# Optimization experiments

Hardware: AMD Instinct MI355X
Metric: run time of the kernel (lower is better)

The kernel has to match this reference:

```python
import jax, jax.numpy as jnp
import numpy as np

V = 1048576        # number of leaves (power of two -> uniform tree depth)
EMB = 128
B = 65536
DEPTH = int(np.log2(V))  # 20: every leaf of the complete heap sits at depth 20


def setup_inputs() -> dict:
    key = jax.random.key(0)
    k1, k2, k3, k4 = jax.random.split(key, 4)
    emb_table = jax.random.normal(k1, (V, EMB), dtype=jnp.float32)
    hsoftmax = jax.random.uniform(k2, (V - 1, EMB), dtype=jnp.float32)  # torch.rand init
    u = jax.random.randint(k3, (B,), 0, V, dtype=jnp.int32)
    v = jax.random.randint(k4, (B,), 0, V, dtype=jnp.int32)
    return {"emb_table": emb_table, "hsoftmax": hsoftmax, "u": u, "v": v}


def _paths(u):
    """Root-to-leaf path (visited as leaf-to-root) for leaf u.
    Returns path_nodes [B, DEPTH] (inner-node indices) and
    path_signs [B, DEPTH] (+1 if we arrived as a left child, -1 otherwise)."""
    node = (V - 1) + u  # heap index of leaf; leaf_pos is the identity
    nodes, signs = [], []
    for _ in range(DEPTH):  # fixed depth: static Python loop, jit-friendly
        is_left = (node & 1) == 1
        parent = jnp.where(is_left, node >> 1, (node - 1) >> 1)
        nodes.append(parent)
        signs.append(jnp.where(is_left, 1.0, -1.0).astype(jnp.float32))
        node = parent
    return jnp.stack(nodes, axis=1), jnp.stack(signs, axis=1)


def reference(emb_table, hsoftmax, u, v):
    # v_emb: [B, E]
    v_emb = emb_table[v]
    path_nodes, path_signs = _paths(u)          # [B, D], [B, D]
    node_embs = hsoftmax[path_nodes]            # [B, D, E] gather
    dots = jnp.einsum("bde,be->bd", node_embs, v_emb)
    # left child: -log(sigmoid(s)); right child: -log(1-sigmoid(s)) = -log(sigmoid(-s))
    loss = -jnp.sum(jax.nn.log_sigmoid(path_signs * dots), axis=1)  # [B]
    return loss
```

## Files before the change

kernel.cpp:

```cpp
#include <hip/hip_runtime.h>
#include <hip/hip_bf16.h>
#include <math.h>

#define V_LEAVES 1048576
#define EMB 128
#define DEPTH 20

__global__ __launch_bounds__(256, 4) void deepwalk_hsm_kernel(
    const float* __restrict__ emb_table,
    const float* __restrict__ hsoftmax,
    const int*   __restrict__ u,
    const int*   __restrict__ v,
    float*       __restrict__ out,
    int batch)
{
    const int tid  = blockIdx.x * blockDim.x + threadIdx.x;
    const int elem = tid >> 4;
    const int sl   = tid & 15;
    if (elem >= batch) return;

    const int vi = v[elem];
    const float4* vrow = (const float4*)(emb_table + (size_t)vi * EMB);
    const float4 ve0 = vrow[sl * 2 + 0];
    const float4 ve1 = vrow[sl * 2 + 1];

    const unsigned np = (unsigned)V_LEAVES + (unsigned)u[elem];

    {
    }
    unsigned p0 = (np >> 1) - 1u;
    const float4* hrow = (const float4*)(hsoftmax + (size_t)p0 * EMB);
    float4 h0 = hrow[sl * 2 + 0];
    float4 h1 = hrow[sl * 2 + 1];

    float loss = 0.0f;

#pragma unroll 4
    for (int d = 0; d < DEPTH; ++d) {
        const float4 c0 = h0;
        const float4 c1 = h1;

        if (d + 1 < DEPTH) {
            const unsigned pn = (np >> (d + 2)) - 1u;
            const float4* nrow = (const float4*)(hsoftmax + (size_t)pn * EMB);
            h0 = nrow[sl * 2 + 0];
            h1 = nrow[sl * 2 + 1];
        }

        float p = c0.x * ve0.x + c0.y * ve0.y + c0.z * ve0.z + c0.w * ve0.w
                + c1.x * ve1.x + c1.y * ve1.y + c1.z * ve1.z + c1.w * ve1.w;

        p += __shfl_xor(p, 1, 64);
        p += __shfl_xor(p, 2, 64);
        p += __shfl_xor(p, 4, 64);
        p += __shfl_xor(p, 8, 64);

        const bool is_left = ((np >> d) & 1u) == 0u;
        const float x  = is_left ? p : -p;
        const float ax = fabsf(x);
        loss += fmaxf(-x, 0.0f) + log1pf(__expf(-ax));
    }

    if (sl == 0) out[elem] = loss;
}

extern "C" void kernel_launch(void* const* d_in, const int* in_sizes, int n_in,
                              void* d_out, int out_size, void* d_ws, size_t ws_size,
                              hipStream_t stream) {
    const float* emb_table = (const float*)d_in[0];
    const float* hsoftmax  = (const float*)d_in[1];
    const int*   u         = (const int*)d_in[2];
    const int*   v         = (const int*)d_in[3];
    float*       out       = (float*)d_out;

    const int batch = in_sizes[2];
    const int threads = batch * 16;
    const int block = 256;
    const int grid = (threads + block - 1) / block;

    deepwalk_hsm_kernel<<<grid, block, 0, stream>>>(
        emb_table, hsoftmax, u, v, out, batch);
}
```

Before: 848.5 us.

## Prefetch path rows in groups of four and share reduction shuffles across dots

Restructures the depth loop into five chunks of four tree levels. It double-buffers the hsoftmax row loads so that four rows are in flight while the previous four are being reduced. The cross-lane reduction is transposed so that four dot products share five shuffles instead of sixteen, and each lane then evaluates the log-sigmoid for one of the four levels. log1pf is replaced by a fast log2 approximation. The intent is more memory-level parallelism and fewer shuffle and transcendental instructions, at the cost of higher register pressure and slightly lower accuracy.

```diff
diff --git a/kernel.cpp b/kernel.cpp
--- a/kernel.cpp
+++ b/kernel.cpp
@@ -20,46 +20,75 @@
     if (elem >= batch) return;
 
     const int vi = v[elem];
-    const float4* vrow = (const float4*)(emb_table + (size_t)vi * EMB);
+    const float4* vrow = (const float4*)(emb_table) + (unsigned)vi * 32u;
     const float4 ve0 = vrow[sl * 2 + 0];
     const float4 ve1 = vrow[sl * 2 + 1];
 
     const unsigned np = (unsigned)V_LEAVES + (unsigned)u[elem];
 
-    {
+    const float4* hbase = (const float4*)hsoftmax;
+
+    float4 hA[4][2], hB[4][2];
+
+#pragma unroll
+    for (int k = 0; k < 4; ++k) {
+        const unsigned pn = (np >> (k + 1)) - 1u;
+        const float4* row = hbase + pn * 32u;
+        hA[k][0] = row[sl * 2 + 0];
+        hA[k][1] = row[sl * 2 + 1];
     }
-    unsigned p0 = (np >> 1) - 1u;
-    const float4* hrow = (const float4*)(hsoftmax + (size_t)p0 * EMB);
-    float4 h0 = hrow[sl * 2 + 0];
-    float4 h1 = hrow[sl * 2 + 1];
 
     float loss = 0.0f;
+    const float LN2 = 0.6931471805599453f;
 
-#pragma unroll 4
-    for (int d = 0; d < DEPTH; ++d) {
-        const float4 c0 = h0;
-        const float4 c1 = h1;
-
-        if (d + 1 < DEPTH) {
-            const unsigned pn = (np >> (d + 2)) - 1u;
-            const float4* nrow = (const float4*)(hsoftmax + (size_t)pn * EMB);
-            h0 = nrow[sl * 2 + 0];
-            h1 = nrow[sl * 2 + 1];
+#pragma unroll
+    for (int c = 0; c < 5; ++c) {
+        if (c < 4) {
+#pragma unroll
+            for (int k = 0; k < 4; ++k) {
+                const int dn = 4 * (c + 1) + k;
+                const unsigned pn = (np >> (dn + 1)) - 1u;
+                const float4* row = hbase + pn * 32u;
+                float4 (&dst)[4][2] = (c & 1) ? hA : hB;
+                dst[k][0] = row[sl * 2 + 0];
+                dst[k][1] = row[sl * 2 + 1];
+            }
         }
 
-        float p = c0.x * ve0.x + c0.y * ve0.y + c0.z * ve0.z + c0.w * ve0.w
-                + c1.x * ve1.x + c1.y * ve1.y + c1.z * ve1.z + c1.w * ve1.w;
+        float4 (&h)[4][2] = (c & 1) ? hB : hA;
 
-        p += __shfl_xor(p, 1, 64);
-        p += __shfl_xor(p, 2, 64);
-        p += __shfl_xor(p, 4, 64);
-        p += __shfl_xor(p, 8, 64);
+        float p[4];
+#pragma unroll
+        for (int k = 0; k < 4; ++k) {
+            const float4 c0 = h[k][0];
+            const float4 c1 = h[k][1];
+            p[k] = c0.x * ve0.x + c0.y * ve0.y + c0.z * ve0.z + c0.w * ve0.w
+                 + c1.x * ve1.x + c1.y * ve1.y + c1.z * ve1.z + c1.w * ve1.w;
+        }
 
+        const int r1 = sl & 1;
+        float a  = r1 ? p[1] : p[0];
+        float b  = r1 ? p[0] : p[1];
+        a += __shfl_xor(b, 1, 64);
+        float e  = r1 ? p[3] : p[2];
+        float f  = r1 ? p[2] : p[3];
+        e += __shfl_xor(f, 1, 64);
+        const int r2 = sl & 2;
+        float r  = r2 ? e : a;
+        float s  = r2 ? a : e;
+        r += __shfl_xor(s, 2, 64);
+        r += __shfl_xor(r, 4, 64);
+        r += __shfl_xor(r, 8, 64);
+
+        const int d = 4 * c + (sl & 3);
         const bool is_left = ((np >> d) & 1u) == 0u;
-        const float x  = is_left ? p : -p;
+        const float x  = is_left ? r : -r;
         const float ax = fabsf(x);
-        loss += fmaxf(-x, 0.0f) + log1pf(__expf(-ax));
+        loss += fmaxf(-x, 0.0f) + LN2 * __log2f(1.0f + __expf(-ax));
     }
+
+    loss += __shfl_xor(loss, 1, 64);
+    loss += __shfl_xor(loss, 2, 64);
 
     if (sl == 0) out[elem] = loss;
 }
```

New measurement: 826.3 us. 1.03x faster.
